# Kernel optimization log

Hardware: AMD Instinct MI355X
Metric: run time of the kernel (lower is better)

Reference implementation:

```python
import jax, jax.numpy as jnp
import numpy as np

N = 65536      # total atoms
D = 1024       # hidden_size (encoder output dim)
H = 2048       # ffn_hidden_size
OUT = 1        # output_size
M = 4096       # number of molecules (segments)


def _lin(k, fi, fo):
    return jax.random.normal(k, (fi, fo), jnp.float32) * (1.0 / np.sqrt(fi))


def setup_inputs() -> dict:
    key = jax.random.key(0)
    ks = jax.random.split(key, 14)
    hidden = jax.random.normal(ks[0], (N, D), jnp.float32)
    segment_ids = jnp.sort(jax.random.randint(ks[1], (N,), 0, M)).astype(jnp.int64)
    inp = {
        "hidden": hidden,
        "ffn_W1": _lin(ks[2], D, H), "ffn_b1": jnp.zeros((H,), jnp.float32),
        "ffn_W2": _lin(ks[3], H, H), "ffn_b2": jnp.zeros((H,), jnp.float32),
        "ffn_W3": _lin(ks[4], H, OUT), "ffn_b3": jnp.zeros((OUT,), jnp.float32),
        "wr_W1": _lin(ks[5], D, H), "wr_b1": jnp.zeros((H,), jnp.float32),
        "wr_W2": _lin(ks[6], H, H), "wr_b2": jnp.zeros((H,), jnp.float32),
        "wr_W3": _lin(ks[7], H, OUT), "wr_b3": jnp.ones((OUT,), jnp.float32),  # bias=1 keeps segment weight sums away from 0
        "segment_ids": segment_ids,
    }
    return inp


def _ffn(x, W1, b1, W2, b2, W3, b3):
    # Dropout(p) is identity in eval; activation = ReLU
    h = jax.nn.relu(x @ W1 + b1)
    h = jax.nn.relu(h @ W2 + b2)
    return h @ W3 + b3


def reference(hidden, ffn_W1, ffn_b1, ffn_W2, ffn_b2, ffn_W3, ffn_b3,
              wr_W1, wr_b1, wr_W2, wr_b2, wr_W3, wr_b3, segment_ids):
    seg = segment_ids.astype(jnp.int32)
    output = _ffn(hidden, ffn_W1, ffn_b1, ffn_W2, ffn_b2, ffn_W3, ffn_b3)   # [N, OUT]
    weights = _ffn(hidden, wr_W1, wr_b1, wr_W2, wr_b2, wr_W3, wr_b3)        # [N, OUT]
    # per-molecule sums over ALL elements of the segment slice (matches .sum())
    out_sum = jax.ops.segment_sum(output.sum(-1), seg, num_segments=M)      # [M]
    w_sum = jax.ops.segment_sum(weights.sum(-1), seg, num_segments=M)       # [M]
    ratio = (out_sum / w_sum)[seg][:, None]                                 # [N, 1]
    return output - weights * ratio
```

## Files before the change

kernel.cpp:

```cpp
#include <hip/hip_runtime.h>
#include <hip/hip_bf16.h>

#define DEVINL __device__ __forceinline__

typedef __attribute__((ext_vector_type(8))) short s8v;
typedef __attribute__((ext_vector_type(4))) float f4v;

using bf16 = __hip_bfloat16;
typedef unsigned short u16;

DEVINL u16 f2bu(float f) {
  bf16 h = __float2bfloat16(f);
  return *reinterpret_cast<u16*>(&h);
}

DEVINL void gload16(const void* g, void* l) {
  __builtin_amdgcn_global_load_lds((const __attribute__((address_space(1))) void*)g,
                                   (__attribute__((address_space(3))) void*)l, 16, 0, 0);
}

#define BAR()   __builtin_amdgcn_s_barrier()
#define LGKM0() asm volatile("s_waitcnt lgkmcnt(0)" ::: "memory")
#define VM(n)   asm volatile("s_waitcnt vmcnt(" #n ")" ::: "memory")

__global__ void k_f32_to_bf16(const float* __restrict__ x, u16* __restrict__ y, long n4) {
  long i = (long)blockIdx.x * blockDim.x + threadIdx.x;
  if (i >= n4) return;
  float4 v = ((const float4*)x)[i];
  ushort4 o;
  o.x = f2bu(v.x); o.y = f2bu(v.y); o.z = f2bu(v.z); o.w = f2bu(v.w);
  ((ushort4*)y)[i] = o;
}

__global__ void k_transpose_bf16(const float* __restrict__ W, u16* __restrict__ Wt,
                                 int rows, int cols) {
  __shared__ float tile[32][33];
  const int tx = threadIdx.x, ty = threadIdx.y;
  const int c0 = blockIdx.x * 32, r0 = blockIdx.y * 32;
  #pragma unroll
  for (int i = ty; i < 32; i += 8)
    tile[i][tx] = W[(long)(r0 + i) * cols + (c0 + tx)];
  __syncthreads();
  #pragma unroll
  for (int i = ty; i < 32; i += 8)
    Wt[(long)(c0 + i) * rows + (r0 + tx)] = f2bu(tile[tx][i]);
}

extern __shared__ char smem[];

template<int EPI>
__global__ __launch_bounds__(512, 2)
void k_gemm8(const u16* __restrict__ A, const u16* __restrict__ Bt,
             u16* __restrict__ C, const float* __restrict__ bias,
             const float* __restrict__ w3, float* __restrict__ oacc,
             int N, int K) {
  const int tid = threadIdx.x;
  const int w = tid >> 6, lane = tid & 63;
  const int id = blockIdx.x;
  const int cpx = gridDim.x >> 3;
  const int sw = (id & 7) * cpx + (id >> 3);
  const int bn = sw & 7, bm = sw >> 3;

  const int wm = (w >> 2) * 128, wn = (w & 3) * 64;
  const int nt = K >> 6;

  f4v acc[8][4];
  #pragma unroll
  for (int i = 0; i < 8; ++i)
    #pragma unroll
    for (int jj = 0; jj < 4; ++jj)
      #pragma unroll
      for (int r = 0; r < 4; ++r) acc[i][jj][r] = 0.f;

  const int rowl = tid >> 2;
  const int jsw = (tid & 3) ^ ((rowl >> 1) & 3);
  const u16* gA = A + (long)(bm * 256 + rowl) * K + jsw * 8;
  const u16* gB = Bt + (long)(bn * 256 + rowl) * K + jsw * 8;
  const long cstr = (long)128 * K;
  const uint wb = (uint)w * 1024u;

  const uint swz = ((uint)((lane >> 4) ^ ((lane >> 1) & 3))) * 16u;
  const uint aoff = (uint)(wm + (lane & 15)) * 64u + swz;
  const uint boff = (uint)(wn + (lane & 15)) * 64u + swz + 32768u;

#define STAGE_A(pp, ks, t) do { \
    const u16* g_ = gA + (long)(t) * 64 + (ks) * 32; \
    char* l_ = smem + (uint)(pp) * 65536u + (uint)(ks) * 16384u + wb; \
    gload16(g_, l_); gload16(g_ + cstr, l_ + 8192); } while (0)
#define STAGE_B(pp, ks, t) do { \
    const u16* g_ = gB + (long)(t) * 64 + (ks) * 32; \
    char* l_ = smem + (uint)(pp) * 65536u + 32768u + (uint)(ks) * 16384u + wb; \
    gload16(g_, l_); gload16(g_ + 8192 * 0 + cstr, l_ + 8192); } while (0)

#define MFMA8(c0i, c1i) do { \
    __builtin_amdgcn_s_setprio(1); \
    _Pragma("unroll") \
    for (int mi = 0; mi < 8; ++mi) { \
      acc[mi][c0i] = __builtin_amdgcn_mfma_f32_16x16x32_bf16(afr[mi], bfr[0], acc[mi][c0i], 0, 0, 0); \
      acc[mi][c1i] = __builtin_amdgcn_mfma_f32_16x16x32_bf16(afr[mi], bfr[1], acc[mi][c1i], 0, 0, 0); \
    } \
    __builtin_amdgcn_s_setprio(0); } while (0)

  STAGE_A(0, 0, 0); STAGE_B(0, 0, 0); STAGE_A(0, 1, 0); STAGE_B(0, 1, 0);
  if (nt > 1) { STAGE_A(1, 0, 1); STAGE_B(1, 0, 1); VM(4); }
  else        { VM(0); }
  BAR();

  s8v afr[8], bfr[2];
  for (int t = 0; t < nt; ++t) {
    const int p = t & 1, q = p ^ 1;
    const uint pb = (uint)p * 65536u;
    #pragma unroll
    for (int mi = 0; mi < 8; ++mi)
      afr[mi] = *(const s8v*)(smem + pb + aoff + (uint)mi * 1024u);
    bfr[0] = *(const s8v*)(smem + pb + boff);
    bfr[1] = *(const s8v*)(smem + pb + boff + 1024u);
    if (t + 1 < nt) STAGE_A(q, 1, t + 1);
    BAR(); LGKM0();
    MFMA8(0, 1);
    BAR();
    bfr[0] = *(const s8v*)(smem + pb + boff + 2048u);
    bfr[1] = *(const s8v*)(smem + pb + boff + 3072u);
    if (t + 1 < nt) STAGE_B(q, 1, t + 1);
    VM(8);
    BAR(); LGKM0();
    MFMA8(2, 3);
    BAR();
    #pragma unroll
    for (int mi = 0; mi < 8; ++mi)
      afr[mi] = *(const s8v*)(smem + pb + 16384u + aoff + (uint)mi * 1024u);
    bfr[0] = *(const s8v*)(smem + pb + boff + 16384u);
    bfr[1] = *(const s8v*)(smem + pb + boff + 16384u + 1024u);
    if (t + 2 < nt) STAGE_A(p, 0, t + 2);
    BAR(); LGKM0();
    MFMA8(0, 1);
    BAR();
    bfr[0] = *(const s8v*)(smem + pb + boff + 16384u + 2048u);
    bfr[1] = *(const s8v*)(smem + pb + boff + 16384u + 3072u);
    if (t + 2 < nt) { STAGE_B(p, 0, t + 2); VM(8); }
    else            { VM(0); }
    BAR(); LGKM0();
    MFMA8(2, 3);
    BAR();
  }

  const int crow = bm * 256 + wm + ((lane >> 4) << 2);
  const int ccol = bn * 256 + wn + (lane & 15);
  if (EPI == 1) {
    #pragma unroll
    for (int jj = 0; jj < 4; ++jj) {
      const float bb = bias[ccol + jj * 16];
      #pragma unroll
      for (int mi = 0; mi < 8; ++mi)
        #pragma unroll
        for (int r = 0; r < 4; ++r) {
          float v = acc[mi][jj][r] + bb;
          v = v > 0.f ? v : 0.f;
          C[(long)(crow + mi * 16 + r) * N + ccol + jj * 16] = f2bu(v);
        }
    }
  } else {
    float bb[4], ww[4];
    #pragma unroll
    for (int jj = 0; jj < 4; ++jj) { bb[jj] = bias[ccol + jj * 16]; ww[jj] = w3[ccol + jj * 16]; }
    #pragma unroll
    for (int mi = 0; mi < 8; ++mi)
      #pragma unroll
      for (int r = 0; r < 4; ++r) {
        float s = 0.f;
        #pragma unroll
        for (int jj = 0; jj < 4; ++jj) {
          float v = acc[mi][jj][r] + bb[jj];
          v = v > 0.f ? v : 0.f;
          s += v * ww[jj];
        }
        s += __shfl_xor(s, 1, 64);
        s += __shfl_xor(s, 2, 64);
        s += __shfl_xor(s, 4, 64);
        s += __shfl_xor(s, 8, 64);
        if ((lane & 15) == 0) atomicAdd(&oacc[crow + mi * 16 + r], s);
      }
  }
#undef STAGE_A
#undef STAGE_B
#undef MFMA8
}

__global__ void k_detect(const int* __restrict__ seg, int n, int* __restrict__ flag) {
  if (blockIdx.x == 0 && threadIdx.x == 0) flag[0] = (seg[n - 1] == 0) ? 1 : 0;
}

__global__ void k_segsum(const float* __restrict__ oacc, const float* __restrict__ wacc,
                         const int* __restrict__ seg, const int* __restrict__ flag,
                         const float* __restrict__ ob3, const float* __restrict__ wb3,
                         float* __restrict__ osum, float* __restrict__ wsum, int n) {
  int i = blockIdx.x * blockDim.x + threadIdx.x;
  if (i >= n) return;
  int s = flag[0] ? seg[2 * i] : seg[i];
  atomicAdd(&osum[s], oacc[i] + ob3[0]);
  atomicAdd(&wsum[s], wacc[i] + wb3[0]);
}

__global__ void k_final(const float* __restrict__ oacc, const float* __restrict__ wacc,
                        const int* __restrict__ seg, const int* __restrict__ flag,
                        const float* __restrict__ ob3, const float* __restrict__ wb3,
                        const float* __restrict__ osum, const float* __restrict__ wsum,
                        float* __restrict__ out, int n) {
  int i = blockIdx.x * blockDim.x + threadIdx.x;
  if (i >= n) return;
  int s = flag[0] ? seg[2 * i] : seg[i];
  float o = oacc[i] + ob3[0];
  float ww = wacc[i] + wb3[0];
  out[i] = o - ww * (osum[s] / wsum[s]);
}

extern "C" void kernel_launch(void* const* d_in, const int* in_sizes, int n_in,
                              void* d_out, int out_size, void* d_ws, size_t ws_size,
                              hipStream_t stream) {
  constexpr int NA = 65536, D = 1024, H = 2048, M = 4096;
  const float* hidden = (const float*)d_in[0];
  const float* fW1 = (const float*)d_in[1];
  const float* fb1 = (const float*)d_in[2];
  const float* fW2 = (const float*)d_in[3];
  const float* fb2 = (const float*)d_in[4];
  const float* fW3 = (const float*)d_in[5];
  const float* fb3 = (const float*)d_in[6];
  const float* wW1 = (const float*)d_in[7];
  const float* wb1 = (const float*)d_in[8];
  const float* wW2 = (const float*)d_in[9];
  const float* wb2 = (const float*)d_in[10];
  const float* wW3 = (const float*)d_in[11];
  const float* wb3 = (const float*)d_in[12];
  const int* seg = (const int*)d_in[13];
  float* out = (float*)d_out;

  char* ws = (char*)d_ws;
  size_t off = 0;
  auto alloc = [&](size_t bytes) { char* p = ws + off; off += (bytes + 255) & ~(size_t)255; return p; };
  u16* hbf  = (u16*)alloc((size_t)NA * D * 2);
  u16* w1tf = (u16*)alloc((size_t)H * D * 2);
  u16* w1tw = (u16*)alloc((size_t)H * D * 2);
  u16* w2tf = (u16*)alloc((size_t)H * H * 2);
  u16* w2tw = (u16*)alloc((size_t)H * H * 2);
  u16* h1   = (u16*)alloc((size_t)NA * H * 2);
  float* oacc = (float*)alloc((size_t)NA * 4);
  float* wacc = (float*)alloc((size_t)NA * 4);
  float* osum = (float*)alloc((size_t)M * 4);
  float* wsum = (float*)alloc((size_t)M * 4);
  int* flag = (int*)alloc(256);

  hipFuncSetAttribute((const void*)k_gemm8<1>, hipFuncAttributeMaxDynamicSharedMemorySize, 131072);
  hipFuncSetAttribute((const void*)k_gemm8<2>, hipFuncAttributeMaxDynamicSharedMemorySize, 131072);

  k_f32_to_bf16<<<(int)((long)NA * D / 4 / 256), 256, 0, stream>>>(hidden, hbf, (long)NA * D / 4);
  dim3 tb(32, 8);
  k_transpose_bf16<<<dim3(H / 32, D / 32), tb, 0, stream>>>(fW1, w1tf, D, H);
  k_transpose_bf16<<<dim3(H / 32, D / 32), tb, 0, stream>>>(wW1, w1tw, D, H);
  k_transpose_bf16<<<dim3(H / 32, H / 32), tb, 0, stream>>>(fW2, w2tf, H, H);
  k_transpose_bf16<<<dim3(H / 32, H / 32), tb, 0, stream>>>(wW2, w2tw, H, H);

  hipMemsetAsync(oacc, 0, (size_t)((char*)flag - (char*)oacc), stream);
  k_detect<<<1, 64, 0, stream>>>(seg, NA, flag);

  const int nblk = (H / 256) * (NA / 256);
  k_gemm8<1><<<nblk, 512, 131072, stream>>>(hbf, w1tf, h1, fb1, nullptr, nullptr, H, D);
  k_gemm8<2><<<nblk, 512, 131072, stream>>>(h1, w2tf, nullptr, fb2, fW3, oacc, H, H);
  k_gemm8<1><<<nblk, 512, 131072, stream>>>(hbf, w1tw, h1, wb1, nullptr, nullptr, H, D);
  k_gemm8<2><<<nblk, 512, 131072, stream>>>(h1, w2tw, nullptr, wb2, wW3, wacc, H, H);

  k_segsum<<<NA / 256, 256, 0, stream>>>(oacc, wacc, seg, flag, fb3, wb3, osum, wsum, NA);
  k_final<<<NA / 256, 256, 0, stream>>>(oacc, wacc, seg, flag, fb3, wb3, osum, wsum, out, NA);
}
```

Baseline: 1.958 ms.

## Double-buffer register fragments and use partial lgkm waits in GEMM main loop

The GEMM inner loop now keeps two sets of A and B register fragments, so LDS reads for the next sub-step are issued before the current MFMA block runs. Full lgkmcnt(0) waits become partial lgkmcnt(n) waits, and several barriers are dropped so LDS reads overlap with matrix math. The global-to-LDS vmcnt waits are also reordered. This raises register pressure, and the hand-counted wait values make the correctness of the synchronisation fragile.

```diff
diff --git a/kernel.cpp b/kernel.cpp
--- a/kernel.cpp
+++ b/kernel.cpp
@@ -19,9 +19,9 @@
                                    (__attribute__((address_space(3))) void*)l, 16, 0, 0);
 }
 
-#define BAR()   __builtin_amdgcn_s_barrier()
-#define LGKM0() asm volatile("s_waitcnt lgkmcnt(0)" ::: "memory")
-#define VM(n)   asm volatile("s_waitcnt vmcnt(" #n ")" ::: "memory")
+#define BAR()    __builtin_amdgcn_s_barrier()
+#define LGKM(n)  asm volatile("s_waitcnt lgkmcnt(" #n ")" ::: "memory")
+#define VM(n)    asm volatile("s_waitcnt vmcnt(" #n ")" ::: "memory")
 
 __global__ void k_f32_to_bf16(const float* __restrict__ x, u16* __restrict__ y, long n4) {
   long i = (long)blockIdx.x * blockDim.x + threadIdx.x;
@@ -90,58 +90,63 @@
 #define STAGE_B(pp, ks, t) do { \
     const u16* g_ = gB + (long)(t) * 64 + (ks) * 32; \
     char* l_ = smem + (uint)(pp) * 65536u + 32768u + (uint)(ks) * 16384u + wb; \
-    gload16(g_, l_); gload16(g_ + 8192 * 0 + cstr, l_ + 8192); } while (0)
-
-#define MFMA8(c0i, c1i) do { \
+    gload16(g_, l_); gload16(g_ + cstr, l_ + 8192); } while (0)
+
+#define RD_A(dst, base, ksb) do { \
+    _Pragma("unroll") \
+    for (int mi_ = 0; mi_ < 8; ++mi_) \
+      dst[mi_] = *(const s8v*)(smem + (base) + (ksb) + aoff + (uint)mi_ * 1024u); } while (0)
+#define RD_B(dst, base, ksb, c0) do { \
+    dst[0] = *(const s8v*)(smem + (base) + (ksb) + boff + (uint)(c0) * 1024u); \
+    dst[1] = *(const s8v*)(smem + (base) + (ksb) + boff + (uint)((c0) + 1) * 1024u); } while (0)
+
+#define MFMA8(A_, B_, c0i, c1i) do { \
     __builtin_amdgcn_s_setprio(1); \
     _Pragma("unroll") \
-    for (int mi = 0; mi < 8; ++mi) { \
-      acc[mi][c0i] = __builtin_amdgcn_mfma_f32_16x16x32_bf16(afr[mi], bfr[0], acc[mi][c0i], 0, 0, 0); \
-      acc[mi][c1i] = __builtin_amdgcn_mfma_f32_16x16x32_bf16(afr[mi], bfr[1], acc[mi][c1i], 0, 0, 0); \
+    for (int mi_ = 0; mi_ < 8; ++mi_) { \
+      acc[mi_][c0i] = __builtin_amdgcn_mfma_f32_16x16x32_bf16(A_[mi_], B_[0], acc[mi_][c0i], 0, 0, 0); \
+      acc[mi_][c1i] = __builtin_amdgcn_mfma_f32_16x16x32_bf16(A_[mi_], B_[1], acc[mi_][c1i], 0, 0, 0); \
     } \
     __builtin_amdgcn_s_setprio(0); } while (0)
 
+  s8v a0[8], a1[8], b01[2], b23[2];
+
   STAGE_A(0, 0, 0); STAGE_B(0, 0, 0); STAGE_A(0, 1, 0); STAGE_B(0, 1, 0);
-  if (nt > 1) { STAGE_A(1, 0, 1); STAGE_B(1, 0, 1); VM(4); }
-  else        { VM(0); }
+  if (nt > 1) { STAGE_A(1, 0, 1); STAGE_B(1, 0, 1); VM(8); }
+  else        { VM(4); }
   BAR();
-
-  s8v afr[8], bfr[2];
+  RD_A(a0, 0u, 0u); RD_B(b01, 0u, 0u, 0);
+
   for (int t = 0; t < nt; ++t) {
     const int p = t & 1, q = p ^ 1;
-    const uint pb = (uint)p * 65536u;
-    #pragma unroll
-    for (int mi = 0; mi < 8; ++mi)
-      afr[mi] = *(const s8v*)(smem + pb + aoff + (uint)mi * 1024u);
-    bfr[0] = *(const s8v*)(smem + pb + boff);
-    bfr[1] = *(const s8v*)(smem + pb + boff + 1024u);
+    const uint pb = (uint)p * 65536u, qb = (uint)q * 65536u;
+    RD_B(b23, pb, 0u, 2);
     if (t + 1 < nt) STAGE_A(q, 1, t + 1);
-    BAR(); LGKM0();
-    MFMA8(0, 1);
+    BAR(); LGKM(2);
+    MFMA8(a0, b01, 0, 1);
+    if (t + 1 < nt) { VM(6); } else { VM(0); }
     BAR();
-    bfr[0] = *(const s8v*)(smem + pb + boff + 2048u);
-    bfr[1] = *(const s8v*)(smem + pb + boff + 3072u);
+    RD_A(a1, pb, 16384u); RD_B(b01, pb, 16384u, 0);
     if (t + 1 < nt) STAGE_B(q, 1, t + 1);
-    VM(8);
-    BAR(); LGKM0();
-    MFMA8(2, 3);
-    BAR();
-    #pragma unroll
-    for (int mi = 0; mi < 8; ++mi)
-      afr[mi] = *(const s8v*)(smem + pb + 16384u + aoff + (uint)mi * 1024u);
-    bfr[0] = *(const s8v*)(smem + pb + boff + 16384u);
-    bfr[1] = *(const s8v*)(smem + pb + boff + 16384u + 1024u);
+    LGKM(10);
+    MFMA8(a0, b23, 2, 3);
+    RD_B(b23, pb, 16384u, 2);
     if (t + 2 < nt) STAGE_A(p, 0, t + 2);
-    BAR(); LGKM0();
-    MFMA8(0, 1);
-    BAR();
-    bfr[0] = *(const s8v*)(smem + pb + boff + 16384u + 2048u);
-    bfr[1] = *(const s8v*)(smem + pb + boff + 16384u + 3072u);
-    if (t + 2 < nt) { STAGE_B(p, 0, t + 2); VM(8); }
-    else            { VM(0); }
-    BAR(); LGKM0();
-    MFMA8(2, 3);
-    BAR();
+    BAR(); LGKM(2);
+    MFMA8(a1, b01, 0, 1);
+    if (t + 2 < nt) {
+      STAGE_B(p, 0, t + 2);
+      VM(8); BAR();
+      RD_A(a0, qb, 0u); RD_B(b01, qb, 0u, 0);
+      LGKM(10);
+    } else if (t + 1 < nt) {
+      VM(4); BAR();
+      RD_A(a0, qb, 0u); RD_B(b01, qb, 0u, 0);
+      LGKM(10);
+    } else {
+      BAR(); LGKM(0);
+    }
+    MFMA8(a1, b23, 2, 3);
   }
 
   const int crow = bm * 256 + wm + ((lane >> 4) << 2);
@@ -183,6 +188,8 @@
   }
 #undef STAGE_A
 #undef STAGE_B
+#undef RD_A
+#undef RD_B
 #undef MFMA8
 }
 
```

Result: no change. 1.936 ms (-1.2%).
